# Kernel optimization log

Measured on AMD Instinct MI355X. Metric: run time of the kernel, lower is better.

The kernel has to match this reference:

```python
import jax, jax.numpy as jnp
import numpy as np

B, N, D = 2, 2048, 768
H = 12
HD = D // H
SCALE = HD ** -0.5
EPS = 1e-8


def exp0(v, c):
    # Poincare exponential map at origin: tanh(sqrt(c)||v||) * v / (sqrt(c)||v||)
    sc = jnp.sqrt(c)
    n = jnp.sqrt(jnp.sum(v * v, axis=-1, keepdims=True))
    n = jnp.maximum(n, EPS)
    return jnp.tanh(sc * n) * v / (sc * n)


def log0(x, c):
    # Poincare log map at origin: artanh(sqrt(c)||x||) * x / (sqrt(c)||x||)
    sc = jnp.sqrt(c)
    n = jnp.sqrt(jnp.sum(x * x, axis=-1, keepdims=True))
    n = jnp.maximum(n, EPS)
    t = jnp.clip(sc * n, 0.0, 1.0 - 1e-7)
    return jnp.arctanh(t) * x / (sc * n)


def setup_inputs() -> dict:
    key = jax.random.key(0)
    k1, k2, k3 = jax.random.split(key, 3)
    c0 = 0.1
    x = jax.random.normal(k1, (B, N, D), dtype=jnp.float32)
    # rescale so sqrt(c)*||x|| = 0.5 -> valid points strictly inside the ball
    xn = jnp.sqrt(jnp.sum(x * x, axis=-1, keepdims=True))
    x = x * (0.5 / (np.sqrt(c0) * jnp.maximum(xn, EPS)))
    w_qkv = jax.random.normal(k2, (3 * D, D), dtype=jnp.float32) * (D ** -0.5)
    w_proj = jax.random.normal(k3, (D, D), dtype=jnp.float32) * (D ** -0.5)
    b_proj = jnp.zeros((D,), dtype=jnp.float32)
    curvature = jnp.asarray(c0, dtype=jnp.float32)
    return {"x": x, "w_qkv": w_qkv, "w_proj": w_proj, "b_proj": b_proj,
            "curvature": curvature}


def reference(x, w_qkv, w_proj, b_proj, curvature):
    c = curvature
    v = log0(x, c)                                   # [B,N,D] tangent vectors
    qkv = jnp.einsum('bnd,ed->bne', v, w_qkv)        # [B,N,3D]
    qkv = qkv.reshape(B, N, 3, H, HD).transpose(2, 0, 3, 1, 4)  # [3,B,H,N,HD]
    q, k, v_proj = qkv[0], qkv[1], qkv[2]
    # Map q,k back onto the manifold for the hyperbolic distance score
    qm = exp0(q, c)                                  # [B,H,N,HD]
    km = exp0(k, c)
    q_nsq = jnp.sum(qm * qm, axis=-1)                # [B,H,N]
    k_nsq = jnp.sum(km * km, axis=-1)                # [B,H,N]
    dot = jnp.einsum('bhnd,bhmd->bhnm', qm, km)      # [B,H,N,N]
    # ||q-k||^2 = ||q||^2 + ||k||^2 - 2 q.k  (avoids [B,H,N,N,HD] intermediate)
    diff_sq = jnp.maximum(q_nsq[..., :, None] + k_nsq[..., None, :] - 2.0 * dot, 0.0)
    q_cl = jnp.minimum(q_nsq, 0.99)
    k_cl = jnp.minimum(k_nsq, 0.99)
    denom = (1.0 - q_cl)[..., :, None] * (1.0 - k_cl)[..., None, :] + 1e-8
    inner = jnp.maximum(1.0 + 2.0 * diff_sq / denom, 1.0 + 1e-7)
    distances = jnp.arccosh(inner)                   # [B,H,N,N]
    scores = -distances * SCALE
    attn = jax.nn.softmax(scores, axis=-1)
    out = jnp.einsum('bhnm,bhmd->bhnd', attn, v_proj)
    out = out.transpose(0, 2, 1, 3).reshape(B, N, D)
    v_out = jnp.einsum('bnd,ed->bne', out, w_proj) + b_proj
    return exp0(v_out, c)                            # [B,N,D] on manifold
```

## Files before the change

kernel.cpp:

```cpp
#include <hip/hip_runtime.h>
#include <cmath>

#define ROWS 4096
#define DIM 768
#define QKV_COLS 2304
#define NHEAD 12
#define HEAD_DIM 64
#define SEQ 2048

static constexpr float EPS_F = 1e-8f;

typedef __bf16 bfrag __attribute__((ext_vector_type(8)));
typedef float  f32x4 __attribute__((ext_vector_type(4)));

__device__ __forceinline__ float wave_sum64(float v) {
#pragma unroll
  for (int off = 1; off < 64; off <<= 1) v += __shfl_xor(v, off, 64);
  return v;
}

__device__ __forceinline__ unsigned short f2bf(float f) {
  unsigned u = __float_as_uint(f);
  u += 0x7fffu + ((u >> 16) & 1u);
  return (unsigned short)(u >> 16);
}

__device__ __forceinline__ float tanh_over_x(float x) {
  const float e  = __builtin_amdgcn_exp2f(x * 2.8853900817779268f);
  const float th = (e - 1.0f) * __builtin_amdgcn_rcpf(e + 1.0f);
  return (x < 1e-4f) ? 1.0f : th * __builtin_amdgcn_rcpf(x);
}

__device__ __forceinline__ void gl_lds16(const void* g, void* l) {
  __builtin_amdgcn_global_load_lds((const __attribute__((address_space(1))) void*)g,
                                   (__attribute__((address_space(3))) void*)l, 16, 0, 0);
}

__global__ __launch_bounds__(256) void log0_conv(const float* __restrict__ x,
                                                 const float* __restrict__ cptr,
                                                 unsigned short* __restrict__ vout,
                                                 const float* __restrict__ wa, int na,
                                                 const float* __restrict__ wb, int nb,
                                                 unsigned short* __restrict__ da,
                                                 unsigned short* __restrict__ db) {
  if (blockIdx.x >= ROWS / 4) {
    const int i = ((blockIdx.x - ROWS / 4) * 256 + threadIdx.x) * 4;
    const float* s;
    unsigned short* d;
    int j;
    if (i < na) { s = wa; d = da; j = i; }
    else { j = i - na; if (j >= nb) return; s = wb; d = db; }
    const float4 v = *(const float4*)(s + j);
    ushort4 o;
    o.x = f2bf(v.x); o.y = f2bf(v.y); o.z = f2bf(v.z); o.w = f2bf(v.w);
    *(ushort4*)(d + j) = o;
    return;
  }
  const int lane = threadIdx.x & 63;
  const int row  = (blockIdx.x << 2) + (threadIdx.x >> 6);
  const float* xr = x + (size_t)row * DIM;
  unsigned short* vr = vout + (size_t)row * DIM;
  float vals[12];
  float ss = 0.f;
#pragma unroll
  for (int i = 0; i < 12; ++i) {
    float t = xr[lane + (i << 6)];
    vals[i] = t;
    ss += t * t;
  }
  ss = wave_sum64(ss);
  const float sc  = sqrtf(cptr[0]);
  const float n   = fmaxf(sqrtf(ss), EPS_F);
  const float scn = sc * n;
  const float t   = fminf(scn, 1.0f - 1e-7f);
  const float ath = 0.34657359027997264f *
                    __builtin_amdgcn_logf((1.0f + t) * __builtin_amdgcn_rcpf(1.0f - t));
  const float f   = (scn < 1e-4f) ? 1.0f : ath * __builtin_amdgcn_rcpf(scn);
#pragma unroll
  for (int i = 0; i < 12; ++i) vr[lane + (i << 6)] = f2bf(vals[i] * f);
}

__global__ __launch_bounds__(256) void exp0_out_kernel(const float* __restrict__ vin,
                                                       const float* __restrict__ cptr,
                                                       float* __restrict__ outp) {
  const int lane = threadIdx.x & 63;
  const int row  = (blockIdx.x << 2) + (threadIdx.x >> 6);
  const float* vr = vin + (size_t)row * DIM;
  float* orow = outp + (size_t)row * DIM;
  float vals[12];
  float ss = 0.f;
#pragma unroll
  for (int i = 0; i < 12; ++i) {
    float t = vr[lane + (i << 6)];
    vals[i] = t;
    ss += t * t;
  }
  ss = wave_sum64(ss);
  const float sc = sqrtf(cptr[0]);
  const float n  = fmaxf(sqrtf(ss), EPS_F);
  const float f  = tanh_over_x(sc * n);
#pragma unroll
  for (int i = 0; i < 12; ++i) orow[lane + (i << 6)] = vals[i] * f;
}

template<int BM, int BN>
__global__ __launch_bounds__(256) void gemm_nt_dbuf(const unsigned short* __restrict__ A,
                                                    const unsigned short* __restrict__ B,
                                                    float* __restrict__ C,
                                                    int M, int Ncols, int K,
                                                    const float* __restrict__ bias) {
  constexpr int FI = BM / 32;
  constexpr int FJ = BN / 32;
  constexpr int CH = BM / 64;
  __shared__ unsigned short As[2][BM * 32];
  __shared__ unsigned short Bs[2][BN * 32];
  const int tid = threadIdx.x;
  const int w = tid >> 6, lane = tid & 63;
  const int lq = lane & 15, quad = lane >> 4;
  const int wr = w >> 1, wc = w & 1;
  const int row0 = blockIdx.y * BM;
  const int col0 = blockIdx.x * BN;
  const int srow  = lane >> 2;
  const int skoff = (lane & 3) << 3;

  f32x4 acc[FI][FJ];
#pragma unroll
  for (int i = 0; i < FI; ++i)
#pragma unroll
    for (int j = 0; j < FJ; ++j) acc[i][j] = (f32x4){0.f, 0.f, 0.f, 0.f};

  auto pf = [&](int k0, int buf) {
#pragma unroll
    for (int c = 0; c < CH; ++c) {
      const int r = c * 64 + w * 16;
      gl_lds16(A + (size_t)(row0 + r + srow) * K + k0 + skoff, &As[buf][r * 32]);
      gl_lds16(B + (size_t)(col0 + r + srow) * K + k0 + skoff, &Bs[buf][r * 32]);
    }
  };

  pf(0, 0);
  const int NIT = K / 32;
  for (int it = 0; it < NIT; ++it) {
    const int buf = it & 1;
    __syncthreads();
    if (it + 1 < NIT) pf((it + 1) * 32, buf ^ 1);

    bfrag af[FI], bfg[FJ];
#pragma unroll
    for (int i = 0; i < FI; ++i)
      af[i] = *(const bfrag*)&As[buf][(wr * (BM / 2) + i * 16 + lq) * 32 + (quad << 3)];
#pragma unroll
    for (int j = 0; j < FJ; ++j)
      bfg[j] = *(const bfrag*)&Bs[buf][(wc * (BN / 2) + j * 16 + lq) * 32 + (quad << 3)];
#pragma unroll
    for (int i = 0; i < FI; ++i)
#pragma unroll
      for (int j = 0; j < FJ; ++j)
        acc[i][j] = __builtin_amdgcn_mfma_f32_16x16x32_bf16(af[i], bfg[j], acc[i][j], 0, 0, 0);
  }

#pragma unroll
  for (int i = 0; i < FI; ++i) {
    const int crow = row0 + wr * (BM / 2) + i * 16 + (quad << 2);
#pragma unroll
    for (int j = 0; j < FJ; ++j) {
      const int col = col0 + wc * (BN / 2) + j * 16 + lq;
      const float bj = bias ? bias[col] : 0.0f;
      float* cp = C + (size_t)crow * Ncols + col;
#pragma unroll
      for (int r = 0; r < 4; ++r)
        cp[(size_t)r * Ncols] = acc[i][j][r] + bj;
    }
  }
}

__global__ __launch_bounds__(256) void gemm_qkv_fused(const unsigned short* __restrict__ A,
                                                      const unsigned short* __restrict__ B,
                                                      const float* __restrict__ cptr,
                                                      unsigned short* __restrict__ qh,
                                                      unsigned short* __restrict__ kh,
                                                      unsigned short* __restrict__ vth,
                                                      float* __restrict__ qnA,
                                                      float* __restrict__ qnB,
                                                      float* __restrict__ knA,
                                                      float* __restrict__ knB) {
  __shared__ unsigned short As[2][128 * 32];
  __shared__ unsigned short Bs[2][128 * 32];
  const int tid = threadIdx.x;
  const int w = tid >> 6, lane = tid & 63;
  const int lq = lane & 15, quad = lane >> 4;
  const int wr = w >> 1, wc = w & 1;
  const int row0 = blockIdx.y << 7;
  const int col0 = blockIdx.x << 7;
  const int srow  = lane >> 2;
  const int skoff = (lane & 3) << 3;

  f32x4 acc[4][4];
#pragma unroll
  for (int i = 0; i < 4; ++i)
#pragma unroll
    for (int j = 0; j < 4; ++j) acc[i][j] = (f32x4){0.f, 0.f, 0.f, 0.f};

  auto pf = [&](int k0, int buf) {
#pragma unroll
    for (int c = 0; c < 2; ++c) {
      const int r = c * 64 + w * 16;
      gl_lds16(A + (size_t)(row0 + r + srow) * DIM + k0 + skoff, &As[buf][r * 32]);
      gl_lds16(B + (size_t)(col0 + r + srow) * DIM + k0 + skoff, &Bs[buf][r * 32]);
    }
  };

  pf(0, 0);
  for (int it = 0; it < DIM / 32; ++it) {
    const int buf = it & 1;
    __syncthreads();
    if (it + 1 < DIM / 32) pf((it + 1) * 32, buf ^ 1);

    bfrag af[4], bfg[4];
#pragma unroll
    for (int i = 0; i < 4; ++i)
      af[i] = *(const bfrag*)&As[buf][((wr << 6) + (i << 4) + lq) * 32 + (quad << 3)];
#pragma unroll
    for (int j = 0; j < 4; ++j)
      bfg[j] = *(const bfrag*)&Bs[buf][((wc << 6) + (j << 4) + lq) * 32 + (quad << 3)];
#pragma unroll
    for (int i = 0; i < 4; ++i)
#pragma unroll
      for (int j = 0; j < 4; ++j)
        acc[i][j] = __builtin_amdgcn_mfma_f32_16x16x32_bf16(af[i], bfg[j], acc[i][j], 0, 0, 0);
  }

  const int colw = col0 + (wc << 6);
  const int seg  = colw / DIM;
  const int hh   = (colw % DIM) >> 6;
  const int rowb = row0 + (wr << 6);

  if (seg == 2) {
#pragma unroll
    for (int i = 0; i < 4; ++i)
#pragma unroll
      for (int r = 0; r < 4; ++r) {
        const int rowg = rowb + (i << 4) + (quad << 2) + r;
        const int bh = (rowg >> 11) * NHEAD + hh;
        const int n_ = rowg & 2047;
#pragma unroll
        for (int j = 0; j < 4; ++j)
          vth[((size_t)bh * HEAD_DIM + (j << 4) + lq) * SEQ + n_] = f2bf(acc[i][j][r]);
      }
  } else {
    unsigned short* dst = seg ? kh : qh;
    float* nA = seg ? knA : qnA;
    float* nB = seg ? knB : qnB;
    const float sc = sqrtf(cptr[0]);
#pragma unroll
    for (int i = 0; i < 4; ++i)
#pragma unroll
      for (int r = 0; r < 4; ++r) {
        float ss = acc[i][0][r] * acc[i][0][r];
        ss = fmaf(acc[i][1][r], acc[i][1][r], ss);
        ss = fmaf(acc[i][2][r], acc[i][2][r], ss);
        ss = fmaf(acc[i][3][r], acc[i][3][r], ss);
        ss += __shfl_xor(ss, 1, 64);
        ss += __shfl_xor(ss, 2, 64);
        ss += __shfl_xor(ss, 4, 64);
        ss += __shfl_xor(ss, 8, 64);
        const float nn = fmaxf(sqrtf(ss), EPS_F);
        const float f  = tanh_over_x(sc * nn);
        const int rowg = rowb + (i << 4) + (quad << 2) + r;
        const int bh = (rowg >> 11) * NHEAD + hh;
        const int n_ = rowg & 2047;
        unsigned short* rp = dst + ((size_t)bh * SEQ + n_) * HEAD_DIM;
#pragma unroll
        for (int j = 0; j < 4; ++j)
          rp[(j << 4) + lq] = f2bf(acc[i][j][r] * f);
        if (lq == 0) {
          const float nrm = ss * f * f;
          nA[(size_t)bh * SEQ + n_] = nrm;
          nB[(size_t)bh * SEQ + n_] = 1.0f / (1.0f - fminf(nrm, 0.99f));
        }
      }
  }
}

__global__ __launch_bounds__(512, 6) void flash_mfma(const unsigned short* __restrict__ qh,
                                                     const unsigned short* __restrict__ kh,
                                                     const unsigned short* __restrict__ vth,
                                                     const float* __restrict__ qnA,
                                                     const float* __restrict__ qnB,
                                                     const float* __restrict__ knA,
                                                     const float* __restrict__ knB,
                                                     unsigned short* __restrict__ attn_out) {
  const int flat = blockIdx.x;
  const int bhid = flat % 24;
  const int qt   = flat / 24;
  const int h = bhid % NHEAD, b = bhid / NHEAD;
  const int bh = b * NHEAD + h;
  const int tid = threadIdx.x;
  const int w = tid >> 6, lane = tid & 63;
  const int lq = lane & 15, quad = lane >> 4;
  const int wq = w & 3;
  const int wh = w >> 2;

  __shared__ __align__(16) unsigned short Ks[2][2][32 * 64];
  __shared__ __align__(16) unsigned short Vt[2][2][64 * 32];
  __shared__ __align__(16) unsigned short Ps[8][16 * 32];

  const unsigned short* qbase = qh + ((size_t)bh * SEQ + (size_t)qt * 64) * HEAD_DIM;
  const float* knAb = knA + (size_t)bh * SEQ;
  const float* knBb = knB + (size_t)bh * SEQ;
  const char* khb = (const char*)(kh + (size_t)bh * SEQ * HEAD_DIM);
  const char* vtb = (const char*)(vth + (size_t)bh * HEAD_DIM * SEQ);

  const int krow = lane >> 3;
  const int koff = ((wq << 3) + krow) * 128 + (((lane & 7) ^ krow) << 4);
  const int c     = (wq << 6) + lane;
  const int vrow2 = c >> 3;
  const int vd    = (vrow2 << 1) + ((c >> 2) & 1);
  const int vg    = (c & 3) ^ (vrow2 & 3);
  const size_t voffb = (size_t)vd * (SEQ * 2);

  auto prefetch = [&](int kt, int buf) {
    const int kb = (wh << 10) + (kt << 5);
    gl_lds16(khb + (size_t)kb * 128 + koff, (char*)&Ks[wh][buf][0] + (wq << 10));
    gl_lds16(vtb + voffb + (size_t)(kb + (vg << 3)) * 2, (char*)&Vt[wh][buf][0] + (wq << 10));
  };

  bfrag aq[2];
#pragma unroll
  for (int khf = 0; khf < 2; ++khf)
    aq[khf] = *(const bfrag*)(qbase + (size_t)((wq << 4) + lq) * HEAD_DIM + khf * 32 + quad * 8);

  const float qnS = qnA[(size_t)bh * SEQ + qt * 64 + (wq << 4) + lq];
  const float rqS = 2.0f * qnB[(size_t)bh * SEQ + qt * 64 + (wq << 4) + lq];

  bfrag ones;
#pragma unroll
  for (int j = 0; j < 8; ++j) ones[j] = (__bf16)1.0f;

  f32x4 oacc[4];
  f32x4 lacc = (f32x4){0.f, 0.f, 0.f, 0.f};
#pragma unroll
  for (int d = 0; d < 4; ++d) oacc[d] = (f32x4){0.f, 0.f, 0.f, 0.f};
  const int swz = lq & 7;
  const int vsw = (lq >> 1) & 3;
  const int psx = ((lq >> 2) & 3) << 3;

  prefetch(0, 0);
  for (int kt = 0; kt < 32; ++kt) {
    const int buf = kt & 1;
    const int key0 = (wh << 10) + (kt << 5);
    __syncthreads();
    if (kt + 1 < 32) prefetch(kt + 1, buf ^ 1);

    f32x4 kna[2], knr[2];
#pragma unroll
    for (int st = 0; st < 2; ++st) {
      kna[st] = *(const f32x4*)(knAb + key0 + st * 16 + (quad << 2));
      knr[st] = *(const f32x4*)(knBb + key0 + st * 16 + (quad << 2));
    }

    f32x4 s[2];
#pragma unroll
    for (int st = 0; st < 2; ++st) s[st] = (f32x4){0.f, 0.f, 0.f, 0.f};
#pragma unroll
    for (int khf = 0; khf < 2; ++khf)
#pragma unroll
      for (int st = 0; st < 2; ++st) {
        const bfrag ak = *(const bfrag*)&Ks[wh][buf][(st * 16 + lq) * 64 + (((khf << 2) + quad) ^ swz) * 8];
        s[st] = __builtin_amdgcn_mfma_f32_16x16x32_bf16(ak, aq[khf], s[st], 0, 0, 0);
      }

#pragma unroll
    for (int st = 0; st < 2; ++st) {
      unsigned u[4];
#pragma unroll
      for (int i = 0; i < 4; ++i) {
        float tt = fmaf(-2.0f, s[st][i], qnS + kna[st][i]);
        tt = fmaxf(tt, 0.0f);
        const float inner = fmaf(tt, rqS * knr[st][i], 1.0f);
        const float root = __builtin_amdgcn_sqrtf(fmaf(inner, inner, -1.0f));
        const float wgt = __builtin_amdgcn_exp2f(-0.125f * __builtin_amdgcn_logf(inner + root));
        u[i] = __float_as_uint(wgt);
      }
      uint2 pk;
      pk.x = __builtin_amdgcn_perm(u[1], u[0], 0x07060302u);
      pk.y = __builtin_amdgcn_perm(u[3], u[2], 0x07060302u);
      *(uint2*)&Ps[w][(lq << 5) + (((st << 4) + (quad << 2)) ^ psx)] = pk;
    }

    const bfrag ap = *(const bfrag*)&Ps[w][(lq << 5) + ((quad << 3) ^ psx)];
    lacc = __builtin_amdgcn_mfma_f32_16x16x32_bf16(ap, ones, lacc, 0, 0, 0);
#pragma unroll
    for (int d = 0; d < 4; ++d) {
      const int dd = (d << 4) + lq;
      const bfrag bv = *(const bfrag*)&Vt[wh][buf][(dd >> 1) * 64 + (dd & 1) * 32 + (quad ^ vsw) * 8];
      oacc[d] = __builtin_amdgcn_mfma_f32_16x16x32_bf16(ap, bv, oacc[d], 0, 0, 0);
    }
  }

  __syncthreads();
  float* cb = (float*)&Ks[0][0][0];
  float* lb = (float*)&Vt[0][0][0];
  const int ci = (wq << 6) + lane;
  if (wh) {
    float* p = cb + ci * 16;
#pragma unroll
    for (int d = 0; d < 4; ++d) *(f32x4*)(p + (d << 2)) = oacc[d];
    *(f32x4*)(lb + (ci << 2)) = lacc;
  }
  __syncthreads();
  if (wh) return;

  {
    const float* p = cb + ci * 16;
#pragma unroll
    for (int d = 0; d < 4; ++d) oacc[d] += *(const f32x4*)(p + (d << 2));
    lacc += *(const f32x4*)(lb + (ci << 2));
  }

  float rl4[4];
#pragma unroll
  for (int i = 0; i < 4; ++i) rl4[i] = __builtin_amdgcn_rcpf(lacc[i]);

  unsigned short* ob = attn_out + ((size_t)b * SEQ + (size_t)qt * 64 + (wq << 4)) * DIM + h * HEAD_DIM;
#pragma unroll
  for (int d = 0; d < 4; ++d)
#pragma unroll
    for (int i = 0; i < 4; ++i)
      ob[(size_t)(quad * 4 + i) * DIM + d * 16 + lq] = f2bf(oacc[d][i] * rl4[i]);
}

extern "C" void kernel_launch(void* const* d_in, const int* in_sizes, int n_in,
                              void* d_out, int out_size, void* d_ws, size_t ws_size,
                              hipStream_t stream) {
  const float* x      = (const float*)d_in[0];
  const float* w_qkv  = (const float*)d_in[1];
  const float* w_proj = (const float*)d_in[2];
  const float* b_proj = (const float*)d_in[3];
  const float* curv   = (const float*)d_in[4];
  float* outp = (float*)d_out;

  float* ws = (float*)d_ws;
  unsigned short* v_tan_bf = (unsigned short*)ws;
  unsigned short* attn_bf  = (unsigned short*)ws;
  float* v_out = ws + 1572864;
  unsigned short* qh  = (unsigned short*)(v_out + 3145728);
  unsigned short* kh  = qh + 3145728;
  unsigned short* vth = kh + 3145728;
  unsigned short* wqkv_bf  = vth + 3145728;
  unsigned short* wproj_bf = wqkv_bf + 1769472;
  float* qnA = (float*)(wproj_bf + 589824);
  float* qnB = qnA + 49152;
  float* knA = qnB + 49152;
  float* knB = knA + 49152;

  log0_conv<<<dim3(ROWS / 4 + 2304), dim3(256), 0, stream>>>(
      x, curv, v_tan_bf, w_qkv, 1769472, w_proj, 589824, wqkv_bf, wproj_bf);
  gemm_qkv_fused<<<dim3(QKV_COLS / 128, ROWS / 128), dim3(256), 0, stream>>>(
      v_tan_bf, wqkv_bf, curv, qh, kh, vth, qnA, qnB, knA, knB);
  flash_mfma<<<dim3(768), dim3(512), 0, stream>>>(qh, kh, vth, qnA, qnB, knA, knB, attn_bf);
  gemm_nt_dbuf<64, 64><<<dim3(DIM / 64, ROWS / 64), dim3(256), 0, stream>>>(
      attn_bf, wproj_bf, v_out, ROWS, DIM, DIM, b_proj);
  exp0_out_kernel<<<dim3(ROWS / 4), dim3(256), 0, stream>>>(v_out, curv, outp);
}
```

Measured before the change: 197.1 us.

## Triple-buffer K/V tiles and pass P fragments via ds_bpermute instead of LDS

The attention kernel moves from double to triple buffering of the K and V tiles, prefetching two tiles ahead and waiting with an explicit s_waitcnt vmcnt(2) plus a raw s_barrier instead of __syncthreads. The probability tile is no longer written to and read back from a per-wave LDS scratch array. Instead the MFMA A-operand is built from registers using ds_bpermute cross-lane shuffles. This aims to hide more global-load latency and to drop the LDS round trip for P. In exchange it uses more LDS for K/V and relies on hand-set wait counts.

```diff
diff --git a/kernel.cpp b/kernel.cpp
--- a/kernel.cpp
+++ b/kernel.cpp
@@ -12,6 +12,7 @@
 
 typedef __bf16 bfrag __attribute__((ext_vector_type(8)));
 typedef float  f32x4 __attribute__((ext_vector_type(4)));
+typedef unsigned u32x4 __attribute__((ext_vector_type(4)));
 
 __device__ __forceinline__ float wave_sum64(float v) {
 #pragma unroll
@@ -301,9 +302,8 @@
   const int wq = w & 3;
   const int wh = w >> 2;
 
-  __shared__ __align__(16) unsigned short Ks[2][2][32 * 64];
-  __shared__ __align__(16) unsigned short Vt[2][2][64 * 32];
-  __shared__ __align__(16) unsigned short Ps[8][16 * 32];
+  __shared__ __align__(16) unsigned short Ks[3][2][32 * 64];
+  __shared__ __align__(16) unsigned short Vt[3][2][64 * 32];
 
   const unsigned short* qbase = qh + ((size_t)bh * SEQ + (size_t)qt * 64) * HEAD_DIM;
   const float* knAb = knA + (size_t)bh * SEQ;
@@ -321,8 +321,8 @@
 
   auto prefetch = [&](int kt, int buf) {
     const int kb = (wh << 10) + (kt << 5);
-    gl_lds16(khb + (size_t)kb * 128 + koff, (char*)&Ks[wh][buf][0] + (wq << 10));
-    gl_lds16(vtb + voffb + (size_t)(kb + (vg << 3)) * 2, (char*)&Vt[wh][buf][0] + (wq << 10));
+    gl_lds16(khb + (size_t)kb * 128 + koff, (char*)&Ks[buf][wh][0] + (wq << 10));
+    gl_lds16(vtb + voffb + (size_t)(kb + (vg << 3)) * 2, (char*)&Vt[buf][wh][0] + (wq << 10));
   };
 
   bfrag aq[2];
@@ -343,14 +343,19 @@
   for (int d = 0; d < 4; ++d) oacc[d] = (f32x4){0.f, 0.f, 0.f, 0.f};
   const int swz = lq & 7;
   const int vsw = (lq >> 1) & 3;
-  const int psx = ((lq >> 2) & 3) << 3;
+
+  const int adrA = ((((quad << 1) & 3) << 4) | lq) << 2;
+  const int adrB = (((((quad << 1) + 1) & 3) << 4) | lq) << 2;
+  const bool qlo = quad < 2;
 
   prefetch(0, 0);
+  prefetch(1, 1);
+  int bufc = 0;
   for (int kt = 0; kt < 32; ++kt) {
-    const int buf = kt & 1;
     const int key0 = (wh << 10) + (kt << 5);
-    __syncthreads();
-    if (kt + 1 < 32) prefetch(kt + 1, buf ^ 1);
+    asm volatile("s_waitcnt vmcnt(2)" ::: "memory");
+    __builtin_amdgcn_s_barrier();
+    __builtin_amdgcn_sched_barrier(0);
 
     f32x4 kna[2], knr[2];
 #pragma unroll
@@ -358,6 +363,12 @@
       kna[st] = *(const f32x4*)(knAb + key0 + st * 16 + (quad << 2));
       knr[st] = *(const f32x4*)(knBb + key0 + st * 16 + (quad << 2));
     }
+    __builtin_amdgcn_sched_barrier(0);
+
+    if (kt + 2 < 32) {
+      const int bufn = bufc >= 1 ? bufc - 1 : bufc + 2;
+      prefetch(kt + 2, bufn);
+    }
 
     f32x4 s[2];
 #pragma unroll
@@ -366,10 +377,11 @@
     for (int khf = 0; khf < 2; ++khf)
 #pragma unroll
       for (int st = 0; st < 2; ++st) {
-        const bfrag ak = *(const bfrag*)&Ks[wh][buf][(st * 16 + lq) * 64 + (((khf << 2) + quad) ^ swz) * 8];
+        const bfrag ak = *(const bfrag*)&Ks[bufc][wh][(st * 16 + lq) * 64 + (((khf << 2) + quad) ^ swz) * 8];
         s[st] = __builtin_amdgcn_mfma_f32_16x16x32_bf16(ak, aq[khf], s[st], 0, 0, 0);
       }
 
+    unsigned pk[4];
 #pragma unroll
     for (int st = 0; st < 2; ++st) {
       unsigned u[4];
@@ -382,40 +394,56 @@
         const float wgt = __builtin_amdgcn_exp2f(-0.125f * __builtin_amdgcn_logf(inner + root));
         u[i] = __float_as_uint(wgt);
       }
-      uint2 pk;
-      pk.x = __builtin_amdgcn_perm(u[1], u[0], 0x07060302u);
-      pk.y = __builtin_amdgcn_perm(u[3], u[2], 0x07060302u);
-      *(uint2*)&Ps[w][(lq << 5) + (((st << 4) + (quad << 2)) ^ psx)] = pk;
-    }
-
-    const bfrag ap = *(const bfrag*)&Ps[w][(lq << 5) + ((quad << 3) ^ psx)];
+      pk[st * 2 + 0] = __builtin_amdgcn_perm(u[1], u[0], 0x07060302u);
+      pk[st * 2 + 1] = __builtin_amdgcn_perm(u[3], u[2], 0x07060302u);
+    }
+
+    u32x4 pr;
+    {
+      const unsigned a0 = (unsigned)__builtin_amdgcn_ds_bpermute(adrA, (int)pk[0]);
+      const unsigned a1 = (unsigned)__builtin_amdgcn_ds_bpermute(adrA, (int)pk[2]);
+      pr.x = qlo ? a0 : a1;
+      const unsigned b0 = (unsigned)__builtin_amdgcn_ds_bpermute(adrA, (int)pk[1]);
+      const unsigned b1 = (unsigned)__builtin_amdgcn_ds_bpermute(adrA, (int)pk[3]);
+      pr.y = qlo ? b0 : b1;
+      const unsigned c0 = (unsigned)__builtin_amdgcn_ds_bpermute(adrB, (int)pk[0]);
+      const unsigned c1 = (unsigned)__builtin_amdgcn_ds_bpermute(adrB, (int)pk[2]);
+      pr.z = qlo ? c0 : c1;
+      const unsigned d0 = (unsigned)__builtin_amdgcn_ds_bpermute(adrB, (int)pk[1]);
+      const unsigned d1 = (unsigned)__builtin_amdgcn_ds_bpermute(adrB, (int)pk[3]);
+      pr.w = qlo ? d0 : d1;
+    }
+    const bfrag ap = __builtin_bit_cast(bfrag, pr);
+
     lacc = __builtin_amdgcn_mfma_f32_16x16x32_bf16(ap, ones, lacc, 0, 0, 0);
 #pragma unroll
     for (int d = 0; d < 4; ++d) {
       const int dd = (d << 4) + lq;
-      const bfrag bv = *(const bfrag*)&Vt[wh][buf][(dd >> 1) * 64 + (dd & 1) * 32 + (quad ^ vsw) * 8];
+      const bfrag bv = *(const bfrag*)&Vt[bufc][wh][(dd >> 1) * 64 + (dd & 1) * 32 + (quad ^ vsw) * 8];
       oacc[d] = __builtin_amdgcn_mfma_f32_16x16x32_bf16(ap, bv, oacc[d], 0, 0, 0);
     }
+
+    bufc = bufc == 2 ? 0 : bufc + 1;
   }
 
   __syncthreads();
-  float* cb = (float*)&Ks[0][0][0];
-  float* lb = (float*)&Vt[0][0][0];
+  float* cbuf = (float*)&Ks[0][0][0];
+  float* lbuf = (float*)&Vt[0][0][0];
   const int ci = (wq << 6) + lane;
   if (wh) {
-    float* p = cb + ci * 16;
+    float* p = cbuf + ci * 16;
 #pragma unroll
     for (int d = 0; d < 4; ++d) *(f32x4*)(p + (d << 2)) = oacc[d];
-    *(f32x4*)(lb + (ci << 2)) = lacc;
+    *(f32x4*)(lbuf + (ci << 2)) = lacc;
   }
   __syncthreads();
   if (wh) return;
 
   {
-    const float* p = cb + ci * 16;
+    const float* p = cbuf + ci * 16;
 #pragma unroll
     for (int d = 0; d < 4; ++d) oacc[d] += *(const f32x4*)(p + (d << 2));
-    lacc += *(const f32x4*)(lb + (ci << 2));
+    lacc += *(const f32x4*)(lbuf + (ci << 2));
   }
 
   float rl4[4];
```

New measurement: 202.2 us. 1.03x slower.
